# Kernel tuning notes

Measured on AMD Instinct MI355X. Metric: run time of the kernel, lower is better.

Reference implementation:

```python
import jax, jax.numpy as jnp
import numpy as np

F_IN, F_H, N_A, N_B = 256, 512, 40, 4
N_GRAPHS, NODES_PER_GRAPH = 4096, 32
N_NODES = N_GRAPHS * NODES_PER_GRAPH
D_OUT = N_B + N_B * N_A  # 164
BN_EPS = 1e-5


def setup_inputs() -> dict:
    key = jax.random.key(0)
    ks = jax.random.split(key, 8)
    X = jax.random.normal(ks[0], (N_NODES, F_IN), dtype=jnp.float32)
    # fixed-size graphs: consistent NX / NX_rep pair
    NX = jnp.full((N_GRAPHS,), NODES_PER_GRAPH, dtype=jnp.int64)
    NX_rep = jnp.repeat(jnp.arange(N_GRAPHS, dtype=jnp.int64), NODES_PER_GRAPH)
    def kaiming(k, fo, fi):
        return jax.random.normal(k, (fo, fi), dtype=jnp.float32) * np.float32(1.0 / np.sqrt(fi))
    return {
        "X": X, "NX": NX, "NX_rep": NX_rep,
        "W_h": kaiming(ks[1], F_H, 2 * F_IN),          # linear_h (no bias)
        "g_h": jnp.ones((F_H,), jnp.float32), "b_h": jnp.zeros((F_H,), jnp.float32),
        "W_ht": kaiming(ks[2], F_H, F_IN),              # linear_h_t (no bias)
        "g_ht": jnp.ones((F_H,), jnp.float32), "b_ht": jnp.zeros((F_H,), jnp.float32),
        "W_x": kaiming(ks[3], D_OUT, F_H) * 0.1,        # linear_x
        "b_x": jnp.zeros((D_OUT,), jnp.float32),
        "W_xt": kaiming(ks[4], 1, F_H) * 0.1,           # linear_x_t
        "b_xt": jnp.zeros((1,), jnp.float32),
    }


def _batchnorm(x, gamma, beta):
    # BatchNorm1d in training mode: batch statistics, biased variance
    mean = jnp.mean(x, axis=0)
    var = jnp.var(x, axis=0)
    return (x - mean) * jax.lax.rsqrt(var + BN_EPS) * gamma + beta


def reference(X, NX, NX_rep, W_h, g_h, b_h, W_ht, g_ht, b_ht, W_x, b_x, W_xt, b_xt):
    n_graphs = NX.shape[0]
    # graph-level mean pooling via segment sum  -> [G, F_in]
    X_end = jax.ops.segment_sum(X, NX_rep, num_segments=n_graphs) / NX[:, None].astype(X.dtype)
    # concat node features with gathered graph context -> [N, 2*F_in]
    Xc = jnp.concatenate([X, X_end[NX_rep]], axis=1)
    X_h = jax.nn.relu(_batchnorm(Xc @ W_h.T, g_h, b_h))          # [N, F_h]
    X_h_end = jax.nn.relu(_batchnorm(X_end @ W_ht.T, g_ht, b_ht))  # [G, F_h]
    X_x = jnp.exp(X_h @ W_x.T + b_x)                              # [N, D_OUT]
    X_x_end = jnp.exp(X_h_end @ W_xt.T + b_xt)                    # [G, 1]
    # segmented softmax denominator (per graph, over all nodes x D_OUT + end logit)
    X_sum = jnp.sum(jax.ops.segment_sum(X_x, NX_rep, num_segments=n_graphs),
                    axis=-1, keepdims=True) + X_x_end             # [G, 1]
    X_softmax = X_x / X_sum[NX_rep]                               # [N, D_OUT]
    X_softmax_end = X_x_end / X_sum                               # [G, 1]
    connect = X_softmax[:, :N_B]                                  # [N, N_B]
    append = X_softmax[:, N_B:].reshape(-1, N_A, N_B)             # [N, N_A, N_B]
    end = X_softmax_end.squeeze(-1)                               # [G]
    return (append, connect, end)
```

## Files before the change

kernel.cpp:

```cpp
#include <hip/hip_runtime.h>
#include <hip/hip_bf16.h>

typedef __hip_bfloat16 bf16;
typedef __attribute__((ext_vector_type(8))) short bf16x8;
typedef __attribute__((ext_vector_type(4))) float f32x4;

#define N_NODES   131072
#define N_GRAPHS  4096
#define FIN       256
#define FH        512
#define NPAD      176
#define NREAL     164

#define OFF_XB     0UL
#define OFF_XENDB  67108864UL
#define OFF_W1A    69206016UL
#define OFF_BCAT   69468160UL
#define OFF_WXB    69992448UL
#define OFF_STATS  70172672UL
#define OFF_XXE    70180864UL
#define OFF_CCAT   70197248UL
#define OFF_H      86974464UL

__device__ __forceinline__ void gld_lds16(const void* g, void* l) {
  __builtin_amdgcn_global_load_lds(
      (const __attribute__((address_space(1))) void*)g,
      (__attribute__((address_space(3))) void*)l, 16, 0, 0);
}

__device__ __forceinline__ float bf2f(unsigned short u) {
  unsigned int x = ((unsigned int)u) << 16; float f;
  __builtin_memcpy(&f, &x, 4); return f;
}
__device__ __forceinline__ unsigned short f2bf(float f) {
  bf16 h = __float2bfloat16(f); unsigned short u;
  __builtin_memcpy(&u, &h, 2); return u;
}

__global__ __launch_bounds__(256) void k_wcast(
    const float* __restrict__ W_h, const float* __restrict__ W_ht,
    const float* __restrict__ W_x,
    bf16* __restrict__ W1a, bf16* __restrict__ Bcat, bf16* __restrict__ Wxb,
    float* __restrict__ stats)
{
  int i = blockIdx.x * 256 + threadIdx.x;
  if (i < 2048) stats[i] = 0.f;
  if (i < 512 * 512) {
    int of = i >> 9, ic = i & 511;
    float v = W_h[i];
    if (ic < 256) W1a[of * 256 + ic] = __float2bfloat16(v);
    else          Bcat[of * 256 + (ic - 256)] = __float2bfloat16(v);
  }
  if (i < 512 * 256) Bcat[512 * 256 + i] = __float2bfloat16(W_ht[i]);
  if (i < NPAD * 512) {
    int n = i >> 9;
    Wxb[i] = (n < NREAL) ? __float2bfloat16(W_x[i]) : __float2bfloat16(0.f);
  }
}

__global__ __launch_bounds__(256) void k_xend(
    const float* __restrict__ X, const int* __restrict__ NX,
    bf16* __restrict__ Xb, bf16* __restrict__ X_endb)
{
  int g = blockIdx.x;
  int t = threadIdx.x;
  int cg = t & 63;
  int rg = t >> 6;
  const float* Xg = X + (long)g * 32 * FIN;
  bf16* Xbg = Xb + (long)g * 32 * FIN;
  float4 s = {0.f, 0.f, 0.f, 0.f};
  #pragma unroll
  for (int r = 0; r < 8; ++r) {
    int off = (rg * 8 + r) * FIN + cg * 4;
    float4 v = *(const float4*)(Xg + off);
    s.x += v.x; s.y += v.y; s.z += v.z; s.w += v.w;
    ushort4 u = {f2bf(v.x), f2bf(v.y), f2bf(v.z), f2bf(v.w)};
    *(ushort4*)(Xbg + off) = u;
  }
  __shared__ float4 red[256];
  red[t] = s;
  __syncthreads();
  if (t < 64) {
    float4 a = red[t], b = red[t + 64], c = red[t + 128], d = red[t + 192];
    float inv = 1.f / (float)NX[g];
    float4 m = {(a.x + b.x + c.x + d.x) * inv, (a.y + b.y + c.y + d.y) * inv,
                (a.z + b.z + c.z + d.z) * inv, (a.w + b.w + c.w + d.w) * inv};
    ushort4 u = {f2bf(m.x), f2bf(m.y), f2bf(m.z), f2bf(m.w)};
    *(ushort4*)(X_endb + (long)g * FIN + t * 4) = u;
  }
}

__global__ __launch_bounds__(256, 2) void gemm0(
    const bf16* __restrict__ A, const bf16* __restrict__ B,
    float* __restrict__ Cout, float* __restrict__ s1e, float* __restrict__ s2e)
{
  const int bid = blockIdx.x;
  const int blkM = bid >> 3, blkN = bid & 7;
  const int tid = threadIdx.x;
  const int w = tid >> 6, lane = tid & 63;
  const int wm = w >> 1, wn = w & 1;

  __shared__ __align__(16) bf16 lA[128 * 32];
  __shared__ __align__(16) bf16 lB[128 * 32];
  __shared__ float sred[2][2][128];

  f32x4 acc[4][4] = {};
  const int rS = lane >> 2;
  const int cS = (lane & 3) * 8;
  const long baseA = (long)blkM * 128;
  const long baseB = (long)blkN * 128;

  for (int kk = 0; kk < FIN; kk += 32) {
    #pragma unroll
    for (int c = 0; c < 2; ++c) {
      int chunk = 2 * w + c;
      gld_lds16(A + (baseA + chunk * 16 + rS) * FIN + kk + cS, &lA[chunk * 16 * 32]);
      gld_lds16(B + (baseB + chunk * 16 + rS) * FIN + kk + cS, &lB[chunk * 16 * 32]);
    }
    __syncthreads();
    bf16x8 a8[4], b8[4];
    #pragma unroll
    for (int t = 0; t < 4; ++t) {
      a8[t] = *(const bf16x8*)&lA[(wm * 64 + t * 16 + (lane & 15)) * 32 + (lane >> 4) * 8];
      b8[t] = *(const bf16x8*)&lB[(wn * 64 + t * 16 + (lane & 15)) * 32 + (lane >> 4) * 8];
    }
    #pragma unroll
    for (int tm = 0; tm < 4; ++tm)
      #pragma unroll
      for (int tn = 0; tn < 4; ++tn)
        acc[tm][tn] = __builtin_amdgcn_mfma_f32_16x16x32_bf16(a8[tm], b8[tn], acc[tm][tn], 0, 0, 0);
    __syncthreads();
  }

  const int rowq = (lane >> 4) * 4;
  const int coll = lane & 15;
  float p1[4] = {0.f, 0.f, 0.f, 0.f}, p2[4] = {0.f, 0.f, 0.f, 0.f};
  #pragma unroll
  for (int tm = 0; tm < 4; ++tm)
    #pragma unroll
    for (int tn = 0; tn < 4; ++tn)
      #pragma unroll
      for (int r = 0; r < 4; ++r) {
        long row = baseA + wm * 64 + tm * 16 + rowq + r;
        int col = (int)baseB + wn * 64 + tn * 16 + coll;
        float v = acc[tm][tn][r];
        Cout[row * 1024 + col] = v;
        p1[tn] += v; p2[tn] += v * v;
      }

  if (blkN >= 4) {
    #pragma unroll
    for (int tn = 0; tn < 4; ++tn) {
      float q1 = p1[tn], q2 = p2[tn];
      q1 += __shfl_xor(q1, 16); q1 += __shfl_xor(q1, 32);
      q2 += __shfl_xor(q2, 16); q2 += __shfl_xor(q2, 32);
      if (lane < 16) {
        sred[wm][0][wn * 64 + tn * 16 + lane] = q1;
        sred[wm][1][wn * 64 + tn * 16 + lane] = q2;
      }
    }
    __syncthreads();
    int st = tid >> 7, c = tid & 127;
    float v = sred[0][st][c] + sred[1][st][c];
    atomicAdd((st ? s2e : s1e) + (blkN - 4) * 128 + c, v);
  }
}

__global__ __launch_bounds__(256) void k_xxend(
    const float* __restrict__ Ccat, const float* __restrict__ s1e,
    const float* __restrict__ s2e, const float* __restrict__ g_ht,
    const float* __restrict__ b_ht, const float* __restrict__ Wxt,
    const float* __restrict__ bxt, float* __restrict__ Xxe)
{
  __shared__ float aL[512], cL[512];
  int tid = threadIdx.x;
  #pragma unroll
  for (int i = tid; i < 512; i += 256) {
    float mean = s1e[i] * 2.44140625e-4f;
    float var = s2e[i] * 2.44140625e-4f - mean * mean;
    float a = g_ht[i] / sqrtf(var + 1e-5f);
    aL[i] = a; cL[i] = b_ht[i] - mean * a;
  }
  __syncthreads();
  int w = tid >> 6, lane = tid & 63;
  int g = blockIdx.x * 4 + w;
  const float* h = Ccat + (long)g * 1024 + 512;
  float acc = 0.f;
  #pragma unroll
  for (int i = 0; i < 8; ++i) {
    int j = lane + i * 64;
    float x = fmaxf(aL[j] * h[j] + cL[j], 0.f);
    acc += x * Wxt[j];
  }
  #pragma unroll
  for (int off = 32; off; off >>= 1) acc += __shfl_xor(acc, off);
  if (lane == 0) Xxe[g] = expf(acc + bxt[0]);
}

__global__ __launch_bounds__(256, 2) void gemm1(
    const bf16* __restrict__ Xb, const bf16* __restrict__ W1a,
    const float* __restrict__ Ccat, bf16* __restrict__ H,
    float* __restrict__ s1m, float* __restrict__ s2m)
{
  const int bid = blockIdx.x;
  const int tid = threadIdx.x;
  const int w = tid >> 6, lane = tid & 63;

  __shared__ __align__(16) bf16 lA[64 * 32];
  __shared__ __align__(16) bf16 lB[512 * 32];

  f32x4 acc[4][8] = {};
  const int rS = lane >> 2;
  const int cS = (lane & 3) * 8;
  const long baseA = (long)bid * 64;

  for (int kk = 0; kk < FIN; kk += 32) {
    gld_lds16(Xb + (baseA + w * 16 + rS) * FIN + kk + cS, &lA[w * 16 * 32]);
    #pragma unroll
    for (int o = 0; o < 8; ++o) {
      int chunk = o * 4 + w;
      gld_lds16(W1a + (chunk * 16 + rS) * FIN + kk + cS, &lB[chunk * 16 * 32]);
    }
    __syncthreads();
    bf16x8 a8[4], b8[8];
    #pragma unroll
    for (int t = 0; t < 4; ++t)
      a8[t] = *(const bf16x8*)&lA[(t * 16 + (lane & 15)) * 32 + (lane >> 4) * 8];
    #pragma unroll
    for (int j = 0; j < 8; ++j)
      b8[j] = *(const bf16x8*)&lB[(w * 128 + j * 16 + (lane & 15)) * 32 + (lane >> 4) * 8];
    #pragma unroll
    for (int t = 0; t < 4; ++t)
      #pragma unroll
      for (int j = 0; j < 8; ++j)
        acc[t][j] = __builtin_amdgcn_mfma_f32_16x16x32_bf16(a8[t], b8[j], acc[t][j], 0, 0, 0);
    __syncthreads();
  }

  const int q4 = (lane >> 4) * 4;
  const int coll = lane & 15;
  float ct[2][8];
  #pragma unroll
  for (int a = 0; a < 2; ++a)
    #pragma unroll
    for (int j = 0; j < 8; ++j)
      ct[a][j] = Ccat[(long)(bid * 2 + a) * 1024 + w * 128 + j * 16 + coll];

  float p1[8], p2[8];
  #pragma unroll
  for (int j = 0; j < 8; ++j) { p1[j] = 0.f; p2[j] = 0.f; }

  #pragma unroll
  for (int t = 0; t < 4; ++t)
    #pragma unroll
    for (int j = 0; j < 8; ++j)
      #pragma unroll
      for (int r = 0; r < 4; ++r) {
        long row = baseA + t * 16 + q4 + r;
        int col = w * 128 + j * 16 + coll;
        float h = acc[t][j][r] + ct[t >> 1][j];
        H[row * FH + col] = __float2bfloat16(h);
        p1[j] += h; p2[j] += h * h;
      }

  #pragma unroll
  for (int j = 0; j < 8; ++j) {
    float q1 = p1[j], q2 = p2[j];
    q1 += __shfl_xor(q1, 16); q1 += __shfl_xor(q1, 32);
    q2 += __shfl_xor(q2, 16); q2 += __shfl_xor(q2, 32);
    if (lane < 16) {
      atomicAdd(s1m + w * 128 + j * 16 + lane, q1);
      atomicAdd(s2m + w * 128 + j * 16 + lane, q2);
    }
  }
}

__global__ __launch_bounds__(256, 2) void gemm2(
    const bf16* __restrict__ Hraw, const bf16* __restrict__ Wxb,
    const float* __restrict__ s1m, const float* __restrict__ s2m,
    const float* __restrict__ g_h, const float* __restrict__ b_h,
    const float* __restrict__ b_x, const float* __restrict__ Xxe,
    float* __restrict__ outA, float* __restrict__ outC, float* __restrict__ outE)
{
  const int blk = blockIdx.x;
  const int tid = threadIdx.x;
  const int w = tid >> 6, lane = tid & 63;

  __shared__ __align__(16) bf16 lA[128 * 32];
  __shared__ __align__(16) bf16 lB[NPAD * 32];
  __shared__ float aL[512], cL[512];

  #pragma unroll
  for (int i = tid; i < 512; i += 256) {
    float mean = s1m[i] * 7.62939453125e-6f;
    float var = s2m[i] * 7.62939453125e-6f - mean * mean;
    float a = g_h[i] / sqrtf(var + 1e-5f);
    aL[i] = a; cL[i] = b_h[i] - mean * a;
  }
  __syncthreads();

  f32x4 acc[2][11] = {};
  const int rS = lane >> 2;
  const int cS = (lane & 3) * 8;
  const long baseRow = (long)blk * 128;

  for (int kk = 0; kk < FH; kk += 32) {
    for (int o = w; o < 11; o += 4)
      gld_lds16(Wxb + (o * 16 + rS) * FH + kk + cS, &lB[o * 16 * 32]);

    f32x4 a0 = *(const f32x4*)&aL[kk + cS];
    f32x4 a1 = *(const f32x4*)&aL[kk + cS + 4];
    f32x4 c0 = *(const f32x4*)&cL[kk + cS];
    f32x4 c1 = *(const f32x4*)&cL[kk + cS + 4];
    #pragma unroll
    for (int c = 0; c < 2; ++c) {
      int chunk = 2 * w + c;
      uint4 raw = *(const uint4*)(Hraw + (baseRow + chunk * 16 + rS) * FH + kk + cS);
      unsigned short* u = (unsigned short*)&raw;
      #pragma unroll
      for (int j = 0; j < 4; ++j) {
        float v = bf2f(u[j]);
        u[j] = f2bf(fmaxf(a0[j] * v + c0[j], 0.f));
      }
      #pragma unroll
      for (int j = 0; j < 4; ++j) {
        float v = bf2f(u[4 + j]);
        u[4 + j] = f2bf(fmaxf(a1[j] * v + c1[j], 0.f));
      }
      *(uint4*)&lA[(chunk * 16 + rS) * 32 + cS] = raw;
    }
    __syncthreads();

    bf16x8 a8[2], b8[11];
    #pragma unroll
    for (int t = 0; t < 2; ++t)
      a8[t] = *(const bf16x8*)&lA[(w * 32 + t * 16 + (lane & 15)) * 32 + (lane >> 4) * 8];
    #pragma unroll
    for (int t = 0; t < 11; ++t)
      b8[t] = *(const bf16x8*)&lB[(t * 16 + (lane & 15)) * 32 + (lane >> 4) * 8];
    #pragma unroll
    for (int tm = 0; tm < 2; ++tm)
      #pragma unroll
      for (int tn = 0; tn < 11; ++tn)
        acc[tm][tn] = __builtin_amdgcn_mfma_f32_16x16x32_bf16(a8[tm], b8[tn], acc[tm][tn], 0, 0, 0);
    __syncthreads();
  }

  const int rowq = (lane >> 4) * 4;
  const int coll = lane & 15;
  const int g = blk * 4 + w;
  float psum = 0.f;
  #pragma unroll
  for (int tn = 0; tn < 11; ++tn) {
    int col = tn * 16 + coll;
    bool valid = col < NREAL;
    float bx = valid ? b_x[col] : 0.f;
    #pragma unroll
    for (int tm = 0; tm < 2; ++tm)
      #pragma unroll
      for (int r = 0; r < 4; ++r) {
        float p = valid ? expf(acc[tm][tn][r] + bx) : 0.f;
        acc[tm][tn][r] = p;
        psum += p;
      }
  }
  #pragma unroll
  for (int off = 32; off; off >>= 1) psum += __shfl_xor(psum, off);
  float Xe = Xxe[g];
  float inv = 1.0f / (psum + Xe);
  if (lane == 0) outE[g] = Xe * inv;

  #pragma unroll
  for (int tn = 0; tn < 11; ++tn) {
    int col = tn * 16 + coll;
    if (col >= NREAL) continue;
    #pragma unroll
    for (int tm = 0; tm < 2; ++tm)
      #pragma unroll
      for (int r = 0; r < 4; ++r) {
        long row = baseRow + w * 32 + tm * 16 + rowq + r;
        float v = acc[tm][tn][r] * inv;
        if (col >= 4) outA[row * 160 + (col - 4)] = v;
        else          outC[row * 4 + col] = v;
      }
  }
}

extern "C" void kernel_launch(void* const* d_in, const int* in_sizes, int n_in,
                              void* d_out, int out_size, void* d_ws, size_t ws_size,
                              hipStream_t stream)
{
  const float* X    = (const float*)d_in[0];
  const int*   NX   = (const int*)d_in[1];
  const float* W_h  = (const float*)d_in[3];
  const float* g_h  = (const float*)d_in[4];
  const float* b_h  = (const float*)d_in[5];
  const float* W_ht = (const float*)d_in[6];
  const float* g_ht = (const float*)d_in[7];
  const float* b_ht = (const float*)d_in[8];
  const float* W_x  = (const float*)d_in[9];
  const float* b_x  = (const float*)d_in[10];
  const float* W_xt = (const float*)d_in[11];
  const float* b_xt = (const float*)d_in[12];

  char* ws = (char*)d_ws;
  bf16*  Xb    = (bf16*)(ws + OFF_XB);
  bf16*  X_endb= (bf16*)(ws + OFF_XENDB);
  bf16*  W1a   = (bf16*)(ws + OFF_W1A);
  bf16*  Bcat  = (bf16*)(ws + OFF_BCAT);
  bf16*  Wxb   = (bf16*)(ws + OFF_WXB);
  float* stats = (float*)(ws + OFF_STATS);
  float* s1m = stats, *s2m = stats + 512, *s1e = stats + 1024, *s2e = stats + 1536;
  float* Xxe   = (float*)(ws + OFF_XXE);
  float* Ccat  = (float*)(ws + OFF_CCAT);
  bf16*  H     = (bf16*)(ws + OFF_H);

  float* outA = (float*)d_out;
  float* outC = outA + (long)N_NODES * 160;
  float* outE = outC + (long)N_NODES * 4;

  k_wcast<<<1024, 256, 0, stream>>>(W_h, W_ht, W_x, W1a, Bcat, Wxb, stats);
  k_xend<<<N_GRAPHS, 256, 0, stream>>>(X, NX, Xb, X_endb);
  gemm0<<<256, 256, 0, stream>>>(X_endb, Bcat, Ccat, s1e, s2e);
  k_xxend<<<1024, 256, 0, stream>>>(Ccat, s1e, s2e, g_ht, b_ht, W_xt, b_xt, Xxe);
  gemm1<<<2048, 256, 0, stream>>>(Xb, W1a, Ccat, H, s1m, s2m);
  gemm2<<<1024, 256, 0, stream>>>(H, Wxb, s1m, s2m, g_h, b_h, b_x, Xxe, outA, outC, outE);
}
```

Before: 403.2 us.

## Make gemm1 persistent with LDS-resident weight half and triple-buffered A tiles

gemm1 now runs 256 blocks of 512 threads. Each block loads one 256-column half of W1a into LDS once (128 KB) and loops over 8 row tiles of 128 rows. A tiles are streamed through a 3-stage buffer, prefetched two k-steps ahead with manual vmcnt waits and barriers. This removes the per-block reload of the full weight matrix and overlaps global loads with MFMA work. The costs are large LDS use, which limits occupancy to one block per CU, and only 256 blocks to spread across the CUs.

Result: no change. 399.5 us (-0.9%).

```diff
diff --git a/kernel.cpp b/kernel.cpp
--- a/kernel.cpp
+++ b/kernel.cpp
@@ -197,80 +197,121 @@
   if (lane == 0) Xxe[g] = expf(acc + bxt[0]);
 }
 
-__global__ __launch_bounds__(256, 2) void gemm1(
+#define G1_STEP(MT, KS, WAIT, BAR)                                             \
+  {                                                                            \
+    if (WAIT) asm volatile("s_waitcnt vmcnt(1)" ::: "memory");                 \
+    if (BAR) { __builtin_amdgcn_s_barrier();                                   \
+               asm volatile("" ::: "memory"); }                                \
+    int s2_ = (MT) * 8 + (KS) + 2; if (s2_ > 63) s2_ = 63;                     \
+    gld_lds16(Xb + (rowbase + (long)(s2_ >> 3) * 128 + w * 16 + rS) * FIN      \
+                 + (s2_ & 7) * 32 + cS,                                        \
+              &lAf[ao2 + w * 512]);                                            \
+    if ((KS) == 0) {                                                           \
+      long gb_ = ((long)(mgrp * 8 + (MT))) * 4 + wm * 2;                       \
+      _Pragma("unroll")                                                        \
+      for (int a_ = 0; a_ < 2; ++a_)                                           \
+        _Pragma("unroll")                                                      \
+        for (int j_ = 0; j_ < 4; ++j_)                                         \
+          ct[a_][j_] = Ccat[(gb_ + a_) * 1024 + nhalf * 256 + wn * 64          \
+                            + j_ * 16 + coll];                                 \
+    }                                                                          \
+    bf16x8 a8_[4], b8_[4];                                                     \
+    _Pragma("unroll")                                                          \
+    for (int t_ = 0; t_ < 4; ++t_)                                             \
+      a8_[t_] = *(const bf16x8*)&lAf[ao0 + (wm * 64 + t_ * 16 + coll) * 32     \
+                                     + hi * 8];                                \
+    _Pragma("unroll")                                                          \
+    for (int j_ = 0; j_ < 4; ++j_)                                             \
+      b8_[j_] = *(const bf16x8*)&lW[((KS) * 256 + wn * 64 + j_ * 16 + coll)    \
+                                    * 32 + hi * 8];                            \
+    _Pragma("unroll")                                                          \
+    for (int t_ = 0; t_ < 4; ++t_)                                             \
+      _Pragma("unroll")                                                        \
+      for (int j_ = 0; j_ < 4; ++j_)                                           \
+        acc[t_][j_] = __builtin_amdgcn_mfma_f32_16x16x32_bf16(                 \
+            a8_[t_], b8_[j_], acc[t_][j_], 0, 0, 0);                           \
+    unsigned tmp_ = ao0; ao0 = ao1; ao1 = ao2; ao2 = tmp_;                     \
+  }
+
+__global__ __launch_bounds__(512) void gemm1(
     const bf16* __restrict__ Xb, const bf16* __restrict__ W1a,
     const float* __restrict__ Ccat, bf16* __restrict__ H,
     float* __restrict__ s1m, float* __restrict__ s2m)
 {
   const int bid = blockIdx.x;
+  const int nhalf = bid & 1;
+  const int mgrp  = bid >> 1;
   const int tid = threadIdx.x;
   const int w = tid >> 6, lane = tid & 63;
-
-  __shared__ __align__(16) bf16 lA[64 * 32];
-  __shared__ __align__(16) bf16 lB[512 * 32];
-
-  f32x4 acc[4][8] = {};
+  const int wm = w >> 2, wn = w & 3;
   const int rS = lane >> 2;
   const int cS = (lane & 3) * 8;
-  const long baseA = (long)bid * 64;
-
-  for (int kk = 0; kk < FIN; kk += 32) {
-    gld_lds16(Xb + (baseA + w * 16 + rS) * FIN + kk + cS, &lA[w * 16 * 32]);
-    #pragma unroll
-    for (int o = 0; o < 8; ++o) {
-      int chunk = o * 4 + w;
-      gld_lds16(W1a + (chunk * 16 + rS) * FIN + kk + cS, &lB[chunk * 16 * 32]);
-    }
-    __syncthreads();
-    bf16x8 a8[4], b8[8];
-    #pragma unroll
-    for (int t = 0; t < 4; ++t)
-      a8[t] = *(const bf16x8*)&lA[(t * 16 + (lane & 15)) * 32 + (lane >> 4) * 8];
-    #pragma unroll
-    for (int j = 0; j < 8; ++j)
-      b8[j] = *(const bf16x8*)&lB[(w * 128 + j * 16 + (lane & 15)) * 32 + (lane >> 4) * 8];
-    #pragma unroll
-    for (int t = 0; t < 4; ++t)
-      #pragma unroll
-      for (int j = 0; j < 8; ++j)
-        acc[t][j] = __builtin_amdgcn_mfma_f32_16x16x32_bf16(a8[t], b8[j], acc[t][j], 0, 0, 0);
-    __syncthreads();
-  }
-
-  const int q4 = (lane >> 4) * 4;
+  const int hi = lane >> 4;
   const int coll = lane & 15;
-  float ct[2][8];
-  #pragma unroll
-  for (int a = 0; a < 2; ++a)
-    #pragma unroll
-    for (int j = 0; j < 8; ++j)
-      ct[a][j] = Ccat[(long)(bid * 2 + a) * 1024 + w * 128 + j * 16 + coll];
-
-  float p1[8], p2[8];
-  #pragma unroll
-  for (int j = 0; j < 8; ++j) { p1[j] = 0.f; p2[j] = 0.f; }
-
-  #pragma unroll
-  for (int t = 0; t < 4; ++t)
-    #pragma unroll
-    for (int j = 0; j < 8; ++j)
-      #pragma unroll
-      for (int r = 0; r < 4; ++r) {
-        long row = baseA + t * 16 + q4 + r;
-        int col = w * 128 + j * 16 + coll;
-        float h = acc[t][j][r] + ct[t >> 1][j];
-        H[row * FH + col] = __float2bfloat16(h);
-        p1[j] += h; p2[j] += h * h;
-      }
-
-  #pragma unroll
-  for (int j = 0; j < 8; ++j) {
+  const int rowq = hi * 4;
+
+  __shared__ __align__(16) bf16 lW[8 * 256 * 32];
+  __shared__ __align__(16) bf16 lAf[3 * 128 * 32];
+
+  const long wrow = (long)nhalf * 256;
+  #pragma unroll
+  for (int c0 = 0; c0 < 16; ++c0) {
+    int c = c0 * 8 + w;
+    gld_lds16(W1a + (wrow + (c & 15) * 16 + rS) * FIN + (c >> 4) * 32 + cS,
+              &lW[c * 512]);
+  }
+  const long rowbase = (long)mgrp * 1024;
+  gld_lds16(Xb + (rowbase + w * 16 + rS) * FIN + 0  + cS, &lAf[0    + w * 512]);
+  gld_lds16(Xb + (rowbase + w * 16 + rS) * FIN + 32 + cS, &lAf[4096 + w * 512]);
+  asm volatile("s_waitcnt vmcnt(0)" ::: "memory");
+  __builtin_amdgcn_s_barrier();
+  asm volatile("" ::: "memory");
+
+  f32x4 acc[4][4] = {};
+  float p1[4] = {0.f, 0.f, 0.f, 0.f}, p2[4] = {0.f, 0.f, 0.f, 0.f};
+  unsigned ao0 = 0, ao1 = 4096, ao2 = 8192;
+
+  #pragma unroll 1
+  for (int mt = 0; mt < 8; ++mt) {
+    float ct[2][4];
+    G1_STEP(mt, 0, 0, 0)
+    G1_STEP(mt, 1, 0, 1)
+    G1_STEP(mt, 2, 1, 1)
+    G1_STEP(mt, 3, 1, 1)
+    G1_STEP(mt, 4, 1, 1)
+    G1_STEP(mt, 5, 1, 1)
+    G1_STEP(mt, 6, 1, 1)
+    G1_STEP(mt, 7, 1, 1)
+    asm volatile("s_waitcnt vmcnt(0)" ::: "memory");
+    __builtin_amdgcn_s_barrier();
+    asm volatile("" ::: "memory");
+
+    const long rtile = rowbase + (long)mt * 128 + wm * 64;
+    #pragma unroll
+    for (int t = 0; t < 4; ++t) {
+      #pragma unroll
+      for (int j = 0; j < 4; ++j) {
+        int col = nhalf * 256 + wn * 64 + j * 16 + coll;
+        #pragma unroll
+        for (int r = 0; r < 4; ++r) {
+          float h = acc[t][j][r] + ct[t >> 1][j];
+          H[(rtile + t * 16 + rowq + r) * FH + col] = __float2bfloat16(h);
+          p1[j] += h; p2[j] += h * h;
+        }
+        acc[t][j][0] = 0.f; acc[t][j][1] = 0.f;
+        acc[t][j][2] = 0.f; acc[t][j][3] = 0.f;
+      }
+    }
+  }
+
+  #pragma unroll
+  for (int j = 0; j < 4; ++j) {
     float q1 = p1[j], q2 = p2[j];
     q1 += __shfl_xor(q1, 16); q1 += __shfl_xor(q1, 32);
     q2 += __shfl_xor(q2, 16); q2 += __shfl_xor(q2, 32);
     if (lane < 16) {
-      atomicAdd(s1m + w * 128 + j * 16 + lane, q1);
-      atomicAdd(s2m + w * 128 + j * 16 + lane, q2);
+      atomicAdd(s1m + nhalf * 256 + wn * 64 + j * 16 + lane, q1);
+      atomicAdd(s2m + nhalf * 256 + wn * 64 + j * 16 + lane, q2);
     }
   }
 }
@@ -423,6 +464,6 @@
   k_xend<<<N_GRAPHS, 256, 0, stream>>>(X, NX, Xb, X_endb);
   gemm0<<<256, 256, 0, stream>>>(X_endb, Bcat, Ccat, s1e, s2e);
   k_xxend<<<1024, 256, 0, stream>>>(Ccat, s1e, s2e, g_ht, b_ht, W_xt, b_xt, Xxe);
-  gemm1<<<2048, 256, 0, stream>>>(Xb, W1a, Ccat, H, s1m, s2m);
+  gemm1<<<256, 512, 0, stream>>>(Xb, W1a, Ccat, H, s1m, s2m);
   gemm2<<<1024, 256, 0, stream>>>(H, Wxb, s1m, s2m, g_h, b_h, b_x, Xxe, outA, outC, outE);
 }
```

## Make gemm1 persistent with register-resident weights and per-wave LDS ring

Applied to the files above, without the earlier changes.

gemm1 now launches 256 blocks of 512 threads, and each block processes 512 rows in 8 tiles of 64. Each wave keeps its 64-column slice of W1a (all of K=256) in registers for the whole block, so the weights are no longer reloaded through LDS on every k-step. The X rows stream through a private 4-slot LDS ring per wave, using async global-to-LDS loads issued two steps ahead and explicit vmcnt waits instead of __syncthreads. This is meant to cut weight traffic and barrier stalls. The cost is high register pressure from 32 bf16x8 weight registers plus the accumulators, and only 256 blocks to occupy the GPU, which may leave some compute units idle.

Result: faster. 389.8 us (-3.3%).

```diff
diff --git a/kernel.cpp b/kernel.cpp
--- a/kernel.cpp
+++ b/kernel.cpp
@@ -197,7 +197,7 @@
   if (lane == 0) Xxe[g] = expf(acc + bxt[0]);
 }
 
-__global__ __launch_bounds__(256, 2) void gemm1(
+__global__ __launch_bounds__(512) void gemm1(
     const bf16* __restrict__ Xb, const bf16* __restrict__ W1a,
     const float* __restrict__ Ccat, bf16* __restrict__ H,
     float* __restrict__ s1m, float* __restrict__ s2m)
@@ -205,72 +205,93 @@
   const int bid = blockIdx.x;
   const int tid = threadIdx.x;
   const int w = tid >> 6, lane = tid & 63;
-
-  __shared__ __align__(16) bf16 lA[64 * 32];
-  __shared__ __align__(16) bf16 lB[512 * 32];
-
-  f32x4 acc[4][8] = {};
   const int rS = lane >> 2;
   const int cS = (lane & 3) * 8;
-  const long baseA = (long)bid * 64;
-
-  for (int kk = 0; kk < FIN; kk += 32) {
-    gld_lds16(Xb + (baseA + w * 16 + rS) * FIN + kk + cS, &lA[w * 16 * 32]);
-    #pragma unroll
-    for (int o = 0; o < 8; ++o) {
-      int chunk = o * 4 + w;
-      gld_lds16(W1a + (chunk * 16 + rS) * FIN + kk + cS, &lB[chunk * 16 * 32]);
-    }
-    __syncthreads();
-    bf16x8 a8[4], b8[8];
+  const int hi = lane >> 4;
+  const int coll = lane & 15;
+
+  __shared__ __align__(16) bf16 ring[8][4][2048];
+
+  bf16x8 b8[4][8];
+  #pragma unroll
+  for (int j = 0; j < 4; ++j)
+    #pragma unroll
+    for (int ks = 0; ks < 8; ++ks)
+      b8[j][ks] = *(const bf16x8*)(W1a + (w * 64 + j * 16 + coll) * FIN
+                                   + ks * 32 + hi * 8);
+
+  const long rowbase = (long)bid * 512;
+  #pragma unroll
+  for (int s = 0; s < 2; ++s)
+    #pragma unroll
+    for (int c = 0; c < 4; ++c)
+      gld_lds16(Xb + (rowbase + c * 16 + rS) * FIN + s * 32 + cS,
+                &ring[w][s][c * 512]);
+
+  f32x4 acc[4][4] = {};
+  float p1[4] = {0.f, 0.f, 0.f, 0.f}, p2[4] = {0.f, 0.f, 0.f, 0.f};
+
+  #pragma unroll 1
+  for (int mt = 0; mt < 8; ++mt) {
+    const long g0 = (rowbase >> 5) + mt * 2;
+    float ct[2][4];
+    #pragma unroll
+    for (int a = 0; a < 2; ++a)
+      #pragma unroll
+      for (int j = 0; j < 4; ++j)
+        ct[a][j] = Ccat[(g0 + a) * 1024 + w * 64 + j * 16 + coll];
+
+    #pragma unroll
+    for (int ks = 0; ks < 8; ++ks) {
+      if (ks < 2) asm volatile("s_waitcnt vmcnt(12)" ::: "memory");
+      else        asm volatile("s_waitcnt vmcnt(4)" ::: "memory");
+
+      {
+        int tgt = mt * 8 + ks + 2; if (tgt > 63) tgt = 63;
+        const bf16* src = Xb + (rowbase + (long)(tgt >> 3) * 64 + rS) * FIN
+                          + (tgt & 7) * 32 + cS;
+        #pragma unroll
+        for (int c = 0; c < 4; ++c)
+          gld_lds16(src + c * 16 * FIN, &ring[w][(ks + 2) & 3][c * 512]);
+      }
+
+      bf16x8 a8[4];
+      #pragma unroll
+      for (int t = 0; t < 4; ++t)
+        a8[t] = *(const bf16x8*)&ring[w][ks & 3][(t * 16 + coll) * 32 + hi * 8];
+      #pragma unroll
+      for (int t = 0; t < 4; ++t)
+        #pragma unroll
+        for (int j = 0; j < 4; ++j)
+          acc[t][j] = __builtin_amdgcn_mfma_f32_16x16x32_bf16(
+              a8[t], b8[j][ks], acc[t][j], 0, 0, 0);
+    }
+
+    const long rtile = rowbase + (long)mt * 64;
     #pragma unroll
     for (int t = 0; t < 4; ++t)
-      a8[t] = *(const bf16x8*)&lA[(t * 16 + (lane & 15)) * 32 + (lane >> 4) * 8];
-    #pragma unroll
-    for (int j = 0; j < 8; ++j)
-      b8[j] = *(const bf16x8*)&lB[(w * 128 + j * 16 + (lane & 15)) * 32 + (lane >> 4) * 8];
-    #pragma unroll
-    for (int t = 0; t < 4; ++t)
-      #pragma unroll
-      for (int j = 0; j < 8; ++j)
-        acc[t][j] = __builtin_amdgcn_mfma_f32_16x16x32_bf16(a8[t], b8[j], acc[t][j], 0, 0, 0);
-    __syncthreads();
-  }
-
-  const int q4 = (lane >> 4) * 4;
-  const int coll = lane & 15;
-  float ct[2][8];
-  #pragma unroll
-  for (int a = 0; a < 2; ++a)
-    #pragma unroll
-    for (int j = 0; j < 8; ++j)
-      ct[a][j] = Ccat[(long)(bid * 2 + a) * 1024 + w * 128 + j * 16 + coll];
-
-  float p1[8], p2[8];
-  #pragma unroll
-  for (int j = 0; j < 8; ++j) { p1[j] = 0.f; p2[j] = 0.f; }
-
-  #pragma unroll
-  for (int t = 0; t < 4; ++t)
-    #pragma unroll
-    for (int j = 0; j < 8; ++j)
-      #pragma unroll
-      for (int r = 0; r < 4; ++r) {
-        long row = baseA + t * 16 + q4 + r;
-        int col = w * 128 + j * 16 + coll;
-        float h = acc[t][j][r] + ct[t >> 1][j];
-        H[row * FH + col] = __float2bfloat16(h);
-        p1[j] += h; p2[j] += h * h;
-      }
-
-  #pragma unroll
-  for (int j = 0; j < 8; ++j) {
+      #pragma unroll
+      for (int j = 0; j < 4; ++j) {
+        int col = w * 64 + j * 16 + coll;
+        #pragma unroll
+        for (int r = 0; r < 4; ++r) {
+          float h = acc[t][j][r] + ct[t >> 1][j];
+          H[(rtile + t * 16 + hi * 4 + r) * FH + col] = __float2bfloat16(h);
+          p1[j] += h; p2[j] += h * h;
+        }
+        acc[t][j][0] = 0.f; acc[t][j][1] = 0.f;
+        acc[t][j][2] = 0.f; acc[t][j][3] = 0.f;
+      }
+  }
+
+  #pragma unroll
+  for (int j = 0; j < 4; ++j) {
     float q1 = p1[j], q2 = p2[j];
     q1 += __shfl_xor(q1, 16); q1 += __shfl_xor(q1, 32);
     q2 += __shfl_xor(q2, 16); q2 += __shfl_xor(q2, 32);
     if (lane < 16) {
-      atomicAdd(s1m + w * 128 + j * 16 + lane, q1);
-      atomicAdd(s2m + w * 128 + j * 16 + lane, q2);
+      atomicAdd(s1m + w * 64 + j * 16 + lane, q1);
+      atomicAdd(s2m + w * 64 + j * 16 + lane, q2);
     }
   }
 }
@@ -423,6 +444,6 @@
   k_xend<<<N_GRAPHS, 256, 0, stream>>>(X, NX, Xb, X_endb);
   gemm0<<<256, 256, 0, stream>>>(X_endb, Bcat, Ccat, s1e, s2e);
   k_xxend<<<1024, 256, 0, stream>>>(Ccat, s1e, s2e, g_ht, b_ht, W_xt, b_xt, Xxe);
-  gemm1<<<2048, 256, 0, stream>>>(Xb, W1a, Ccat, H, s1m, s2m);
+  gemm1<<<256, 512, 0, stream>>>(Xb, W1a, Ccat, H, s1m, s2m);
   gemm2<<<1024, 256, 0, stream>>>(H, Wxb, s1m, s2m, g_h, b_h, b_x, Xxe, outA, outC, outE);
 }
```
